# Kernel tuning notes

Hardware: AMD Instinct MI355X
Metric: run time of the kernel (lower is better)

## Reference

```python
import jax, jax.numpy as jnp
import numpy as np

N_NODES = 100000


def gcn_conv(x, src, dst, norm, W, b, n):
    # x: [N, F_in]; src/dst: [E'] (with self loops); norm: [E']
    xw = x @ W                                   # [N, F_out]
    msg = xw[src] * norm[:, None]                # [E', F_out]
    agg = jax.ops.segment_sum(msg, dst, num_segments=n)
    return agg + b


def _self_loops_and_norm(edge_index, n):
    loop = jnp.arange(n, dtype=edge_index.dtype)
    src = jnp.concatenate([edge_index[0], loop])
    dst = jnp.concatenate([edge_index[1], loop])
    deg = jax.ops.segment_sum(jnp.ones_like(dst, dtype=jnp.float32), dst, num_segments=n)
    dis = jnp.where(deg > 0, jax.lax.rsqrt(jnp.maximum(deg, 1.0)), 0.0)
    norm = dis[src] * dis[dst]
    return src, dst, norm


def setup_inputs() -> dict:
    key = jax.random.key(0)
    k1, k2, k3, k4, k5, k6 = jax.random.split(key, 6)
    n, e = N_NODES, 1600000
    f_in, f_hid, f_out = 64, 128, 64
    x = jax.random.normal(k1, (n, f_in), dtype=jnp.float32)
    edge_index = jax.random.randint(k2, (2, e), 0, n, dtype=jnp.int64)
    # Glorot init like PyG GCNConv
    W0 = jax.random.normal(k3, (f_in, f_hid), dtype=jnp.float32) * (1.0 / np.sqrt(f_in))
    b0 = jnp.zeros((f_hid,), dtype=jnp.float32)
    W1 = jax.random.normal(k4, (f_hid, f_out), dtype=jnp.float32) * (1.0 / np.sqrt(f_hid))
    b1 = jnp.zeros((f_out,), dtype=jnp.float32)
    return {"x": x, "edge_index": edge_index, "W0": W0, "b0": b0, "W1": W1, "b1": b1}


def reference(x, edge_index, W0, b0, W1, b1):
    n = x.shape[0]
    src, dst, norm = _self_loops_and_norm(edge_index, n)
    h = gcn_conv(x, src, dst, norm, W0, b0, n)
    h = jax.nn.relu(h)
    out = gcn_conv(h, src, dst, norm, W1, b1, n)
    return jax.nn.sigmoid(out)
```

## Files before the change

kernel.cpp:

```cpp
#include <hip/hip_runtime.h>
#include <hip/hip_fp16.h>
#include <math.h>


#define FIN 64
#define FHID 128
#define FOUT 64
#define NPB 128
#define LOGNPB 7
#define BMAX 800
#define G 128
#define CAP 4096

typedef _Float16 f16x2 __attribute__((ext_vector_type(2)));

#if defined(__has_builtin)
#if __has_builtin(__builtin_amdgcn_fdot2)
#define HAS_FDOT2 1
#endif
#endif

__device__ __forceinline__ float dot2(f16x2 a, f16x2 b, float c) {
#ifdef HAS_FDOT2
    return __builtin_amdgcn_fdot2(a, b, c, false);
#else
    c = fmaf((float)a[0], (float)b[0], c);
    return fmaf((float)a[1], (float)b[1], c);
#endif
}


__global__ __launch_bounds__(256) void khist(const int* __restrict__ dst,
                                             int* __restrict__ ghist,
                                             int e, int B, int chunk) {
    __shared__ int h[BMAX];
    int g = blockIdx.x, t = threadIdx.x;
    for (int i = t; i < B; i += 256) h[i] = 0;
    __syncthreads();
    int lo = g * chunk, hi = min(e, lo + chunk);
    for (int i = lo + t; i < hi; i += 256)
        atomicAdd(&h[dst[i] >> LOGNPB], 1);
    __syncthreads();
    for (int i = t; i < B; i += 256) ghist[i * G + g] = h[i];
}

__global__ __launch_bounds__(256) void kscanA(const int* __restrict__ ghist,
                                              int* __restrict__ gbase,
                                              int* __restrict__ tot, int B) {
    int per = (B + gridDim.x - 1) / gridDim.x;
    int b0 = blockIdx.x * per, b1 = min(B, b0 + per);
    for (int b = b0 + threadIdx.x; b < b1; b += 256) {
        int run = 0;
        #pragma unroll 8
        for (int g = 0; g < G; ++g) {
            int v = ghist[b * G + g];
            gbase[b * G + g] = run;
            run += v;
        }
        tot[b] = run;
    }
}

__global__ __launch_bounds__(256) void kscanB(const int* __restrict__ tot,
                                              int* __restrict__ bb, int B, int e) {
    __shared__ int s[256];
    __shared__ int chunkoff;
    int t = threadIdx.x;
    if (t == 0) chunkoff = 0;
    __syncthreads();
    for (int c0 = 0; c0 < B; c0 += 256) {
        int v = (c0 + t < B) ? tot[c0 + t] : 0;
        s[t] = v;
        __syncthreads();
        for (int off = 1; off < 256; off <<= 1) {
            int u = (t >= off) ? s[t - off] : 0;
            __syncthreads();
            s[t] += u;
            __syncthreads();
        }
        if (c0 + t < B) bb[c0 + t] = s[t] - v + chunkoff;
        __syncthreads();
        if (t == 255) chunkoff += s[255];
        __syncthreads();
    }
    if (t == 0) bb[B] = e;
}

__global__ __launch_bounds__(256) void kscatter(const int* __restrict__ src,
                                                const int* __restrict__ dst,
                                                const int* __restrict__ gbase,
                                                const int* __restrict__ bb,
                                                unsigned* __restrict__ pk,
                                                int e, int B, int chunk) {
    __shared__ int cur[BMAX];
    int g = blockIdx.x, t = threadIdx.x;
    for (int b = t; b < B; b += 256) cur[b] = bb[b] + gbase[b * G + g];
    __syncthreads();
    int lo = g * chunk, hi = min(e, lo + chunk);
    for (int i = lo + t; i < hi; i += 256) {
        int d = dst[i], s = src[i], b = d >> LOGNPB;
        int p = atomicAdd(&cur[b], 1);
        pk[p] = ((unsigned)(d & (NPB - 1)) << 17) | (unsigned)s;
    }
}

__global__ __launch_bounds__(256) void kpsort(const unsigned* __restrict__ pk,
                                              const int* __restrict__ bb,
                                              const float* __restrict__ x,
                                              int* __restrict__ ssrc,
                                              int* __restrict__ rp,
                                              float* __restrict__ dis,
                                              __half* __restrict__ yh,
                                              int n, int e) {
    __shared__ int cnt[NPB];
    __shared__ int pre[NPB];
    __shared__ float disl[NPB];
    __shared__ unsigned stage[CAP];
    int b = blockIdx.x, t = threadIdx.x;
    int lo = bb[b], hi = bb[b + 1], m = hi - lo;
    if (t < NPB) cnt[t] = 0;
    __syncthreads();
    for (int i = lo + t; i < hi; i += 256)
        atomicAdd(&cnt[pk[i] >> 17], 1);
    __syncthreads();
    if (t < NPB) pre[t] = cnt[t];
    __syncthreads();
    #pragma unroll
    for (int off = 1; off < NPB; off <<= 1) {
        int v = (t < NPB && t >= off) ? pre[t - off] : 0;
        __syncthreads();
        if (t < NPB) pre[t] += v;
        __syncthreads();
    }
    if (t < NPB) {
        int node = b * NPB + t;
        int c = cnt[t];
        int bs = lo + pre[t] - c;
        float dv = rsqrtf(1.0f + (float)c);
        disl[t] = dv;
        if (node < n) {
            rp[node] = bs;
            dis[node] = dv;
        }
        cnt[t] = bs - lo;
    }
    if (b == 0 && t == 0) rp[n] = e;
    __syncthreads();
    if (m <= CAP) {
        for (int i = lo + t; i < hi; i += 256) {
            unsigned v = pk[i];
            int p = atomicAdd(&cnt[v >> 17], 1);
            stage[p] = v & 0x1FFFF;
        }
        __syncthreads();
        for (int i = t; i < m; i += 256) ssrc[lo + i] = (int)stage[i];
    } else {
        for (int i = lo + t; i < hi; i += 256) {
            unsigned v = pk[i];
            int p = atomicAdd(&cnt[v >> 17], 1);
            ssrc[lo + p] = (int)(v & 0x1FFFF);
        }
    }
    for (int i = t; i < NPB * 16; i += 256) {
        int node = b * NPB + (i >> 4);
        if (node < n) {
            float d = disl[i >> 4];
            int gi = b * (NPB * 16) + i;
            float4 v = reinterpret_cast<const float4*>(x)[gi];
            __half2 h0, h1;
            h0.x = __float2half(d * v.x); h0.y = __float2half(d * v.y);
            h1.x = __float2half(d * v.z); h1.y = __float2half(d * v.w);
            reinterpret_cast<__half2*>(yh)[gi * 2 + 0] = h0;
            reinterpret_cast<__half2*>(yh)[gi * 2 + 1] = h1;
        }
    }
}

__global__ __launch_bounds__(256) void k_pull16(
        const int* __restrict__ rp, const int* __restrict__ ssrc,
        const float* __restrict__ dis, const __half* __restrict__ yh,
        const float* __restrict__ b1, float* __restrict__ outp,
        __half* __restrict__ outph, int n, int sig) {
    int node4 = blockIdx.x * 4 + (threadIdx.x >> 6);
    if (node4 >= n) return;
    int node = __builtin_amdgcn_readfirstlane(node4);
    int f = threadIdx.x & 63;
    float a0 = __half2float(yh[(size_t)node * 64 + f]);
    float a1 = 0.f, a2 = 0.f, a3 = 0.f, a4 = 0.f, a5 = 0.f, a6 = 0.f, a7 = 0.f;
    int j = rp[node], end = rp[node + 1];
    for (; j + 7 < end; j += 8) {
        int s0 = ssrc[j],     s1 = ssrc[j + 1], s2 = ssrc[j + 2], s3 = ssrc[j + 3];
        int s4 = ssrc[j + 4], s5 = ssrc[j + 5], s6 = ssrc[j + 6], s7 = ssrc[j + 7];
        a0 += __half2float(yh[(size_t)s0 * 64 + f]);
        a1 += __half2float(yh[(size_t)s1 * 64 + f]);
        a2 += __half2float(yh[(size_t)s2 * 64 + f]);
        a3 += __half2float(yh[(size_t)s3 * 64 + f]);
        a4 += __half2float(yh[(size_t)s4 * 64 + f]);
        a5 += __half2float(yh[(size_t)s5 * 64 + f]);
        a6 += __half2float(yh[(size_t)s6 * 64 + f]);
        a7 += __half2float(yh[(size_t)s7 * 64 + f]);
    }
    for (; j + 1 < end; j += 2) {
        int s0 = ssrc[j], s1 = ssrc[j + 1];
        a0 += __half2float(yh[(size_t)s0 * 64 + f]);
        a1 += __half2float(yh[(size_t)s1 * 64 + f]);
    }
    if (j < end)
        a0 += __half2float(yh[(size_t)ssrc[j] * 64 + f]);
    float v = dis[node] * (((a0 + a1) + (a2 + a3)) + ((a4 + a5) + (a6 + a7)));
    if (sig) {
        v += b1[f];
        outp[(size_t)node * 64 + f] = 1.0f / (1.0f + expf(-v));
    } else {
        outph[(size_t)node * 64 + f] = __float2half(v);
    }
}

__global__ __launch_bounds__(256) void k_gemm1(
        const __half* __restrict__ in,
        const float* __restrict__ W0,
        const float* __restrict__ b0,
        __half* __restrict__ h,
        int n, int nwaves) {
    int gw = blockIdx.x * 4 + (threadIdx.x >> 6);
    int lane = threadIdx.x & 63;

    f16x2 w0a[32], w0b[32];
    #pragma unroll
    for (int i = 0; i < 32; ++i) {
        w0a[i] = (f16x2){(_Float16)W0[(2 * i) * FHID + lane],
                         (_Float16)W0[(2 * i + 1) * FHID + lane]};
        w0b[i] = (f16x2){(_Float16)W0[(2 * i) * FHID + 64 + lane],
                         (_Float16)W0[(2 * i + 1) * FHID + 64 + lane]};
    }
    float ba = b0[lane], bbias = b0[64 + lane];

    for (int task = gw; task < n; task += nwaves) {
        int row = __builtin_amdgcn_readfirstlane(task);
        const f16x2* srow = reinterpret_cast<const f16x2*>(in + (size_t)row * FIN);
        float aa = ba, ab = bbias;
        #pragma unroll
        for (int i = 0; i < 32; ++i) {
            f16x2 xv = srow[i];
            aa = dot2(xv, w0a[i], aa);
            ab = dot2(xv, w0b[i], ab);
        }
        h[(size_t)row * FHID + lane]      = __float2half(fmaxf(aa, 0.0f));
        h[(size_t)row * FHID + 64 + lane] = __float2half(fmaxf(ab, 0.0f));
    }
}

__global__ __launch_bounds__(256) void k_gemm2(
        const __half* __restrict__ h,
        const float* __restrict__ W1,
        const float* __restrict__ dis,
        __half* __restrict__ yh,
        int n, int nwaves) {
    int gw = blockIdx.x * 4 + (threadIdx.x >> 6);
    int lane = threadIdx.x & 63;

    f16x2 w1c[64];
    #pragma unroll
    for (int i = 0; i < 64; ++i)
        w1c[i] = (f16x2){(_Float16)W1[(2 * i) * FOUT + lane],
                         (_Float16)W1[(2 * i + 1) * FOUT + lane]};

    for (int task = gw; task < n; task += nwaves) {
        int row = __builtin_amdgcn_readfirstlane(task);
        const f16x2* hrow = reinterpret_cast<const f16x2*>(h + (size_t)row * FHID);
        float acc = 0.0f;
        #pragma unroll
        for (int i = 0; i < 64; ++i)
            acc = dot2(hrow[i], w1c[i], acc);
        yh[(size_t)row * FOUT + lane] = __float2half(dis[row] * acc);
    }
}

extern "C" void kernel_launch(void* const* d_in, const int* in_sizes, int n_in,
                              void* d_out, int out_size, void* d_ws, size_t ws_size,
                              hipStream_t stream) {
    const float* x   = (const float*)d_in[0];
    const int*   ei  = (const int*)d_in[1];
    const float* W0  = (const float*)d_in[2];
    const float* b0  = (const float*)d_in[3];
    const float* W1  = (const float*)d_in[4];
    const float* b1  = (const float*)d_in[5];
    float*       out = (float*)d_out;

    const int n = in_sizes[0] / FIN;
    const int e = in_sizes[1] / 2;
    const int* src = ei;
    const int* dst = ei + e;
    if (n > (1 << 17)) return;

    const int B = (n + NPB - 1) / NPB;
    if (B > BMAX) return;
    const int chunk = (e + G - 1) / G;

    float*    dis  = (float*)d_ws;
    __half*   bufh = (__half*)(dis + n);
    int*      ssrc = (int*)(bufh + (size_t)n * FIN);
    int*      rp   = ssrc + e;
    __half*   yh   = (__half*)(rp + (n + 1));
    char*     region = (char*)(yh + (size_t)n * FIN);
    __half*   hh   = (__half*)region;
    unsigned* pk   = (unsigned*)region;
    int*      ghist = (int*)(pk + e);
    int*      gbase = ghist + (size_t)B * G;
    int*      tot   = gbase + (size_t)B * G;
    int*      bb    = tot + B;
    size_t region_sz = (size_t)n * FHID * sizeof(__half);
    {
        size_t pkchain = (size_t)((char*)(bb + B + 1) - region);
        if (pkchain > region_sz) region_sz = pkchain;
    }
    size_t need = (size_t)(region - (char*)d_ws) + region_sz;
    if (ws_size < need) return;

    khist<<<G, 256, 0, stream>>>(dst, ghist, e, B, chunk);
    kscanA<<<8, 256, 0, stream>>>(ghist, gbase, tot, B);
    kscanB<<<1, 256, 0, stream>>>(tot, bb, B, e);
    kscatter<<<G, 256, 0, stream>>>(src, dst, gbase, bb, pk, e, B, chunk);
    kpsort<<<B, 256, 0, stream>>>(pk, bb, x, ssrc, rp, dis, yh, n, e);

    k_pull16<<<(n + 3) / 4, 256, 0, stream>>>(rp, ssrc, dis, yh, b1,
                                              (float*)nullptr, bufh, n, 0);

    const int blocks = 2048, nwaves = blocks * 4;
    k_gemm1<<<blocks, 256, 0, stream>>>(bufh, W0, b0, hh, n, nwaves);
    k_gemm2<<<blocks, 256, 0, stream>>>(hh, W1, dis, yh, n, nwaves);

    k_pull16<<<(n + 3) / 4, 256, 0, stream>>>(rp, ssrc, dis, yh, b1,
                                              out, (__half*)nullptr, n, 1);
}
```

Measured before the change: 236.9 us.

## Fuse two per-row GEMMs via LDS and sort sources within each destination

The two dense per-row matmul kernels become one kernel. The hidden row is staged in shared memory rather than written to and re-read from a global [N,128] half buffer, which also removes that workspace. Separately, the per-bucket counting sort now keys on destination plus the top two bits of the source index, so neighbor lists come out roughly ordered by source, aiming for better gather locality in the pull kernels. The costs are higher register pressure from holding both weight sets per lane (128 f16x2 values), lower occupancy, and two extra block barriers per iteration.

```diff
diff --git a/kernel.cpp b/kernel.cpp
--- a/kernel.cpp
+++ b/kernel.cpp
@@ -112,18 +112,24 @@
                                               float* __restrict__ dis,
                                               __half* __restrict__ yh,
                                               int n, int e) {
-    __shared__ int cnt[NPB];
+    __shared__ int cnt[NPB * 4];
     __shared__ int pre[NPB];
     __shared__ float disl[NPB];
     __shared__ unsigned stage[CAP];
     int b = blockIdx.x, t = threadIdx.x;
     int lo = bb[b], hi = bb[b + 1], m = hi - lo;
-    if (t < NPB) cnt[t] = 0;
-    __syncthreads();
-    for (int i = lo + t; i < hi; i += 256)
-        atomicAdd(&cnt[pk[i] >> 17], 1);
-    __syncthreads();
-    if (t < NPB) pre[t] = cnt[t];
+    for (int i = t; i < NPB * 4; i += 256) cnt[i] = 0;
+    __syncthreads();
+    for (int i = lo + t; i < hi; i += 256) {
+        unsigned v = pk[i];
+        int key = (int)((v >> 17) << 2) | (int)((v & 0x1FFFF) >> 15);
+        atomicAdd(&cnt[key], 1);
+    }
+    __syncthreads();
+    int tot_t = 0;
+    if (t < NPB)
+        tot_t = cnt[4 * t] + cnt[4 * t + 1] + cnt[4 * t + 2] + cnt[4 * t + 3];
+    if (t < NPB) pre[t] = tot_t;
     __syncthreads();
     #pragma unroll
     for (int off = 1; off < NPB; off <<= 1) {
@@ -134,7 +140,7 @@
     }
     if (t < NPB) {
         int node = b * NPB + t;
-        int c = cnt[t];
+        int c = tot_t;
         int bs = lo + pre[t] - c;
         float dv = rsqrtf(1.0f + (float)c);
         disl[t] = dv;
@@ -142,14 +148,20 @@
             rp[node] = bs;
             dis[node] = dv;
         }
-        cnt[t] = bs - lo;
+        int c0 = cnt[4 * t], c1 = cnt[4 * t + 1], c2 = cnt[4 * t + 2];
+        int run = bs - lo;
+        cnt[4 * t]     = run;
+        cnt[4 * t + 1] = run + c0;
+        cnt[4 * t + 2] = run + c0 + c1;
+        cnt[4 * t + 3] = run + c0 + c1 + c2;
     }
     if (b == 0 && t == 0) rp[n] = e;
     __syncthreads();
     if (m <= CAP) {
         for (int i = lo + t; i < hi; i += 256) {
             unsigned v = pk[i];
-            int p = atomicAdd(&cnt[v >> 17], 1);
+            int key = (int)((v >> 17) << 2) | (int)((v & 0x1FFFF) >> 15);
+            int p = atomicAdd(&cnt[key], 1);
             stage[p] = v & 0x1FFFF;
         }
         __syncthreads();
@@ -157,7 +169,8 @@
     } else {
         for (int i = lo + t; i < hi; i += 256) {
             unsigned v = pk[i];
-            int p = atomicAdd(&cnt[v >> 17], 1);
+            int key = (int)((v >> 17) << 2) | (int)((v & 0x1FFFF) >> 15);
+            int p = atomicAdd(&cnt[key], 1);
             ssrc[lo + p] = (int)(v & 0x1FFFF);
         }
     }
@@ -216,16 +229,20 @@
     }
 }
 
-__global__ __launch_bounds__(256) void k_gemm1(
+__global__ __launch_bounds__(256) void k_mlp(
         const __half* __restrict__ in,
         const float* __restrict__ W0,
         const float* __restrict__ b0,
-        __half* __restrict__ h,
+        const float* __restrict__ W1,
+        const float* __restrict__ dis,
+        __half* __restrict__ yh,
         int n, int nwaves) {
-    int gw = blockIdx.x * 4 + (threadIdx.x >> 6);
-    int lane = threadIdx.x & 63;
-
-    f16x2 w0a[32], w0b[32];
+    __shared__ __half hs[4][FHID];
+    int t = threadIdx.x;
+    int wid = t >> 6, lane = t & 63;
+    int gw = blockIdx.x * 4 + wid;
+
+    f16x2 w0a[32], w0b[32], w1c[64];
     #pragma unroll
     for (int i = 0; i < 32; ++i) {
         w0a[i] = (f16x2){(_Float16)W0[(2 * i) * FHID + lane],
@@ -233,46 +250,41 @@
         w0b[i] = (f16x2){(_Float16)W0[(2 * i) * FHID + 64 + lane],
                          (_Float16)W0[(2 * i + 1) * FHID + 64 + lane]};
     }
-    float ba = b0[lane], bbias = b0[64 + lane];
-
-    for (int task = gw; task < n; task += nwaves) {
-        int row = __builtin_amdgcn_readfirstlane(task);
-        const f16x2* srow = reinterpret_cast<const f16x2*>(in + (size_t)row * FIN);
-        float aa = ba, ab = bbias;
-        #pragma unroll
-        for (int i = 0; i < 32; ++i) {
-            f16x2 xv = srow[i];
-            aa = dot2(xv, w0a[i], aa);
-            ab = dot2(xv, w0b[i], ab);
-        }
-        h[(size_t)row * FHID + lane]      = __float2half(fmaxf(aa, 0.0f));
-        h[(size_t)row * FHID + 64 + lane] = __float2half(fmaxf(ab, 0.0f));
-    }
-}
-
-__global__ __launch_bounds__(256) void k_gemm2(
-        const __half* __restrict__ h,
-        const float* __restrict__ W1,
-        const float* __restrict__ dis,
-        __half* __restrict__ yh,
-        int n, int nwaves) {
-    int gw = blockIdx.x * 4 + (threadIdx.x >> 6);
-    int lane = threadIdx.x & 63;
-
-    f16x2 w1c[64];
     #pragma unroll
     for (int i = 0; i < 64; ++i)
         w1c[i] = (f16x2){(_Float16)W1[(2 * i) * FOUT + lane],
                          (_Float16)W1[(2 * i + 1) * FOUT + lane]};
-
-    for (int task = gw; task < n; task += nwaves) {
-        int row = __builtin_amdgcn_readfirstlane(task);
-        const f16x2* hrow = reinterpret_cast<const f16x2*>(h + (size_t)row * FHID);
-        float acc = 0.0f;
-        #pragma unroll
-        for (int i = 0; i < 64; ++i)
-            acc = dot2(hrow[i], w1c[i], acc);
-        yh[(size_t)row * FOUT + lane] = __float2half(dis[row] * acc);
+    float ba = b0[lane], bbias = b0[64 + lane];
+
+    int gw0 = blockIdx.x * 4;
+    int iters = (n > gw0) ? (n - gw0 + nwaves - 1) / nwaves : 0;
+    for (int it = 0; it < iters; ++it) {
+        int task = gw + it * nwaves;
+        bool act = (task < n);
+        int row = __builtin_amdgcn_readfirstlane(act ? task : 0);
+        if (act) {
+            const f16x2* srow =
+                reinterpret_cast<const f16x2*>(in + (size_t)row * FIN);
+            float aa = ba, ab = bbias;
+            #pragma unroll
+            for (int i = 0; i < 32; ++i) {
+                f16x2 xv = srow[i];
+                aa = dot2(xv, w0a[i], aa);
+                ab = dot2(xv, w0b[i], ab);
+            }
+            hs[wid][lane]      = __float2half(fmaxf(aa, 0.0f));
+            hs[wid][64 + lane] = __float2half(fmaxf(ab, 0.0f));
+        }
+        __syncthreads();
+        if (act) {
+            const f16x2* hrow = reinterpret_cast<const f16x2*>(hs[wid]);
+            float acc = 0.0f;
+            #pragma unroll
+            for (int i = 0; i < 64; ++i)
+                acc = dot2(hrow[i], w1c[i], acc);
+            yh[(size_t)row * FOUT + lane] = __float2half(dis[row] * acc);
+        }
+        __syncthreads();
     }
 }
 
@@ -303,18 +315,12 @@
     int*      rp   = ssrc + e;
     __half*   yh   = (__half*)(rp + (n + 1));
     char*     region = (char*)(yh + (size_t)n * FIN);
-    __half*   hh   = (__half*)region;
     unsigned* pk   = (unsigned*)region;
     int*      ghist = (int*)(pk + e);
     int*      gbase = ghist + (size_t)B * G;
     int*      tot   = gbase + (size_t)B * G;
     int*      bb    = tot + B;
-    size_t region_sz = (size_t)n * FHID * sizeof(__half);
-    {
-        size_t pkchain = (size_t)((char*)(bb + B + 1) - region);
-        if (pkchain > region_sz) region_sz = pkchain;
-    }
-    size_t need = (size_t)(region - (char*)d_ws) + region_sz;
+    size_t need = (size_t)((char*)(bb + B + 1) - (char*)d_ws);
     if (ws_size < need) return;
 
     khist<<<G, 256, 0, stream>>>(dst, ghist, e, B, chunk);
@@ -327,8 +333,7 @@
                                               (float*)nullptr, bufh, n, 0);
 
     const int blocks = 2048, nwaves = blocks * 4;
-    k_gemm1<<<blocks, 256, 0, stream>>>(bufh, W0, b0, hh, n, nwaves);
-    k_gemm2<<<blocks, 256, 0, stream>>>(hh, W1, dis, yh, n, nwaves);
+    k_mlp<<<blocks, 256, 0, stream>>>(bufh, W0, b0, W1, dis, yh, n, nwaves);
 
     k_pull16<<<(n + 3) / 4, 256, 0, stream>>>(rp, ssrc, dis, yh, b1,
                                               out, (__half*)nullptr, n, 1);
```

Result: slower. 315.1 us (+33.0%).
